# Optimization experiments

Measured on AMD Instinct MI355X. Metric: run time of the kernel, lower is better.

The kernel has to match this reference:

```python
import jax, jax.numpy as jnp
import numpy as np

PAD, EOS, SOS = 0, 1, 2
V, E, H, B, T = 32000, 256, 512, 32, 64


def setup_inputs() -> dict:
    key = jax.random.key(0)
    ks = jax.random.split(key, 8)
    s_e = 1.0 / np.sqrt(H)
    emb = jax.random.normal(ks[0], (V, E), dtype=jnp.float32)
    emb = emb.at[PAD].set(0.0)  # padding_idx=PAD
    return {
        "hidden": jax.random.normal(ks[1], (1, B, H), dtype=jnp.float32),
        "emb": emb,
        "W_ih": jax.random.uniform(ks[2], (3 * H, E), minval=-s_e, maxval=s_e, dtype=jnp.float32),
        "W_hh": jax.random.uniform(ks[3], (3 * H, H), minval=-s_e, maxval=s_e, dtype=jnp.float32),
        "b_ih": jax.random.uniform(ks[4], (3 * H,), minval=-s_e, maxval=s_e, dtype=jnp.float32),
        "b_hh": jax.random.uniform(ks[5], (3 * H,), minval=-s_e, maxval=s_e, dtype=jnp.float32),
        "W_proj": jax.random.uniform(ks[6], (V, H), minval=-s_e, maxval=s_e, dtype=jnp.float32),
        "b_proj": jax.random.uniform(ks[7], (V,), minval=-s_e, maxval=s_e, dtype=jnp.float32),
        "max_len": T,
    }


def reference(hidden, emb, W_ih, W_hh, b_ih, b_hh, W_proj, b_proj, max_len):
    # Batched greedy GRU decode, equivalent to Decodeur.generate:
    # per-step: embed -> GRU cell -> linear proj -> argmax, feed back token.
    h0 = hidden[0]                                  # [B, H]
    nb = h0.shape[0]
    y0 = jnp.full((nb,), SOS, dtype=jnp.int32)
    done0 = jnp.zeros((nb,), dtype=bool)

    def step(carry, _):
        h, y, done = carry
        x = emb[y]                                  # [B, E]
        gx = x @ W_ih.T + b_ih                      # [B, 3H]
        gh = h @ W_hh.T + b_hh                      # [B, 3H]
        gxr, gxz, gxn = jnp.split(gx, 3, axis=-1)
        ghr, ghz, ghn = jnp.split(gh, 3, axis=-1)
        r = jax.nn.sigmoid(gxr + ghr)
        z = jax.nn.sigmoid(gxz + ghz)
        n = jnp.tanh(gxn + r * ghn)
        h_new = (1.0 - z) * n + z * h               # [B, H]
        logits = h_new @ W_proj.T + b_proj          # [B, V]
        y_new = jnp.argmax(logits, axis=-1).astype(jnp.int32)
        tok = jnp.where(done, EOS, y_new)           # pad with EOS once finished
        done_new = done | (y_new == EOS)
        return (h_new, tok, done_new), tok

    _, toks = jax.lax.scan(step, (h0, y0, done0), None, length=max_len)
    return toks                                     # [T, B] int32, EOS-padded
```

## Files before the change

kernel.cpp:

```cpp
#include <hip/hip_runtime.h>
#include <math.h>

#define EOS_TOK 1
#define SOS_TOK 2
#define Bn 32
#define Hn 512
#define En 256
#define Vn 32000
#define G3H 1536
#define NBLK 256
#define NTHR 1024
#define VPB 125
#define GPB 6
#define CE 0.0085f
#define LCAP 2048

typedef unsigned long long ull;
typedef unsigned int uint;
typedef __attribute__((ext_vector_type(8))) __bf16 bf16x8;
typedef __attribute__((ext_vector_type(4))) float f32x4;

union U4B { uint4 u; bf16x8 b; };
__device__ __forceinline__ bf16x8 u2b(uint4 u) { U4B x; x.u = u; return x.b; }

#define WBF_OFF 0ull
#define WN_OFF  32768000ull
#define GH_OFF  32896000ull
#define ES_OFF  33092608ull
#define LBS_OFF 33096704ull
#define DN_OFF  33100800ull
#define H_OFF   33101056ull

struct WS {
    unsigned short* wbf; float* wn; float* gh; ull* es; ull* lbs; int* done; float* h;
};
__device__ __forceinline__ WS get_ws(void* p) {
    WS w;
    w.wbf = (unsigned short*)((char*)p + WBF_OFF);
    w.wn  = (float*)((char*)p + WN_OFF);
    w.gh  = (float*)((char*)p + GH_OFF);
    w.es  = (ull*)((char*)p + ES_OFF);
    w.lbs = (ull*)((char*)p + LBS_OFF);
    w.done= (int*)((char*)p + DN_OFF);
    w.h   = (float*)((char*)p + H_OFF);
    return w;
}

template <typename T>
__device__ __forceinline__ T ldA(const T* p) {
    return __hip_atomic_load(p, __ATOMIC_RELAXED, __HIP_MEMORY_SCOPE_AGENT);
}
template <typename T>
__device__ __forceinline__ void stA(T* p, T v) {
    __hip_atomic_store(p, v, __ATOMIC_RELAXED, __HIP_MEMORY_SCOPE_AGENT);
}

struct PadCnt { ull v; ull pad[7]; };
__device__ PadCnt g_leaf[32];
__device__ ull    g_release;

__device__ __forceinline__ void grid_barrier(int bid) {
    __syncthreads();
    if (threadIdx.x == 0) {
        __builtin_amdgcn_s_waitcnt(0);
        ull my = __hip_atomic_fetch_add(&g_leaf[bid >> 3].v, 1ull,
                                        __ATOMIC_RELAXED, __HIP_MEMORY_SCOPE_AGENT) + 1;
        ull k = (my + 7) >> 3;
        if (bid == 0) {
            ull need = k << 3;
            for (;;) {
                bool again = false;
                #pragma unroll
                for (int i = 0; i < 32; ++i) again |= (ldA(&g_leaf[i].v) < need);
                if (!again) break;
                __builtin_amdgcn_s_sleep(1);
            }
            stA(&g_release, k);
        } else {
            while (ldA(&g_release) < k) __builtin_amdgcn_s_sleep(2);
        }
        __asm__ __volatile__("" ::: "memory");
    }
    __syncthreads();
}

__device__ __forceinline__ uint fkey(float f) {
    uint b = __float_as_uint(f);
    return (b & 0x80000000u) ? ~b : (b | 0x80000000u);
}
__device__ __forceinline__ float ifkey(uint k) {
    uint b = (k & 0x80000000u) ? (k ^ 0x80000000u) : ~k;
    return __uint_as_float(b);
}
__device__ __forceinline__ uint f2bf(float f) {
    uint u = __float_as_uint(f);
    return (u + 0x7FFFu + ((u >> 16) & 1u)) >> 16;
}
__device__ __forceinline__ float bflo(uint u) { return __uint_as_float(u << 16); }
__device__ __forceinline__ float bfhi(uint u) { return __uint_as_float(u & 0xFFFF0000u); }
__device__ __forceinline__ float ulo(ull u) { return __uint_as_float((uint)u); }
__device__ __forceinline__ float uhi(ull u) { return __uint_as_float((uint)(u >> 32)); }

struct SM {
    uint4 h4[2048];
    float hn[32];
    float lbv[32];
    float lbv2[32];
    float ghsc[GPB * 32 * 6];
    ull   red[256];
    int   cnt; int pad0[3];
    unsigned short sidx[LCAP];
    float sU[LCAP];
    int   tok[32];
    float gx[192];
};

__device__ void prologue(int tid, int bid, const float* __restrict__ hidden,
                         const float* __restrict__ W_proj, WS w)
{
    for (int i = bid * NTHR + tid; i < Bn * Hn / 2; i += NBLK * NTHR)
        stA((ull*)w.h + i, ((const ull*)hidden)[i]);
    for (int i = bid * NTHR + tid; i < Vn * Hn / 4; i += NBLK * NTHR) {
        float4 v = ((const float4*)W_proj)[i];
        ull o = (ull)(f2bf(v.x) | (f2bf(v.y) << 16))
              | ((ull)(f2bf(v.z) | (f2bf(v.w) << 16)) << 32);
        stA((ull*)w.wbf + i, o);
    }
    for (int r = bid * NTHR + tid; r < Vn; r += NBLK * NTHR) {
        const float4* wr = (const float4*)(W_proj + (size_t)r * Hn);
        float s0 = 0.f, s1 = 0.f;
        for (int e = 0; e < 128; e += 2) {
            float4 a = wr[e], b4 = wr[e + 1];
            s0 += a.x * a.x + a.z * a.z + b4.x * b4.x + b4.z * b4.z;
            s1 += a.y * a.y + a.w * a.w + b4.y * b4.y + b4.w * b4.w;
        }
        stA(&w.wn[r], sqrtf(s0 + s1) * 1.0005f);
    }
}

__device__ void do_gh(int tid, int bid, const float* __restrict__ W_hh,
                      const float* __restrict__ h, SM* sm)
{
    if (tid < 832) return;
    int idx = tid - 832;
    int b = idx & 31, ks = idx >> 5;
    int f40 = ks * 21 + (ks < 2 ? ks : 2);
    int nf4 = 21 + (ks < 2 ? 1 : 0);
    const ull* hp = (const ull*)h + b * 256 + f40 * 2;
    const float4* wr[GPB];
    #pragma unroll
    for (int r6 = 0; r6 < GPB; ++r6)
        wr[r6] = (const float4*)(W_hh + (size_t)(bid * GPB + r6) * Hn) + f40;
    float p[GPB];
    #pragma unroll
    for (int r6 = 0; r6 < GPB; ++r6) p[r6] = 0.f;
    for (int e = 0; e < nf4; ++e) {
        ull u0 = ldA(hp + 2 * e), u1 = ldA(hp + 2 * e + 1);
        float h0 = ulo(u0), h1 = uhi(u0), h2 = ulo(u1), h3 = uhi(u1);
        #pragma unroll
        for (int r6 = 0; r6 < GPB; ++r6) {
            float4 wv4 = wr[r6][e];
            p[r6] += wv4.x * h0 + wv4.y * h1 + wv4.z * h2 + wv4.w * h3;
        }
    }
    #pragma unroll
    for (int r6 = 0; r6 < GPB; ++r6)
        sm->ghsc[(r6 * 32 + b) * 6 + ks] = p[r6];
}
__device__ void fin_gh(int tid, int base, int bid, const float* __restrict__ b_hh,
                       float* __restrict__ gh, SM* sm)
{
    if (tid >= base && tid < base + 192) {
        int idx = tid - base;
        int r6 = idx >> 5, b = idx & 31;
        float s = 0.f;
        #pragma unroll
        for (int j = 0; j < 6; ++j) s += sm->ghsc[(r6 * 32 + b) * 6 + j];
        int r = bid * GPB + r6;
        stA(&gh[(size_t)b * G3H + r], s + b_hh[r]);
    }
}

__device__ __forceinline__ void phase_bc(int tid, int bid, int t, WS w,
                         const float* __restrict__ W_hh, const float* __restrict__ b_hh,
                         const float* __restrict__ W_proj, const float* __restrict__ b_proj,
                         SM* sm)
{
    for (int i = tid; i < 2048; i += NTHR) {
        int bb = i >> 6, e8 = i & 63;
        const ull* hs = (const ull*)w.h + bb * 256 + e8 * 4;
        ull a = ldA(hs), b2 = ldA(hs + 1), c = ldA(hs + 2), d = ldA(hs + 3);
        uint4 P;
        P.x = f2bf(ulo(a))  | (f2bf(uhi(a))  << 16);
        P.y = f2bf(ulo(b2)) | (f2bf(uhi(b2)) << 16);
        P.z = f2bf(ulo(c))  | (f2bf(uhi(c))  << 16);
        P.w = f2bf(ulo(d))  | (f2bf(uhi(d))  << 16);
        sm->h4[(bb << 6) + (e8 ^ bb)] = P;
    }
    __syncthreads();

    do_gh(tid, bid, W_hh, w.h, sm);

    if (tid >= 800 && tid < 832) {
        int b = tid & 31;
        float s = 0.f;
        for (int e8 = 0; e8 < 64; ++e8) {
            uint4 H = sm->h4[(b << 6) + (e8 ^ b)];
            float f0=bflo(H.x),f1=bfhi(H.x),f2=bflo(H.y),f3=bfhi(H.y);
            float f4=bflo(H.z),f5=bfhi(H.z),f6=bflo(H.w),f7=bfhi(H.w);
            s += f0*f0+f1*f1+f2*f2+f3*f3+f4*f4+f5*f5+f6*f6+f7*f7;
        }
        sm->hn[b] = CE * sqrtf(s);
    }

    const int lane = tid & 63, wv = tid >> 6;
    f32x4 c0 = (f32x4){0.f,0.f,0.f,0.f}, c1 = (f32x4){0.f,0.f,0.f,0.f};
    if (wv < 8) {
        int arow = bid * VPB + wv * 16 + (lane & 15);
        if (arow > Vn - 1) arow = Vn - 1;
        const uint4* wp = (const uint4*)w.wbf + (size_t)arow * 64 + (lane >> 4);
        const int bb0 = lane & 15, bb1 = bb0 + 16;
        const int i0 = bb0 << 6, i1 = bb1 << 6;
        const int eb = lane >> 4;
        #pragma unroll
        for (int ks = 0; ks < 16; ++ks) {
            uint4 av = wp[ks * 4];
            int e8 = ks * 4 + eb;
            uint4 b0 = sm->h4[i0 + (e8 ^ bb0)];
            uint4 b1 = sm->h4[i1 + (e8 ^ bb1)];
            c0 = __builtin_amdgcn_mfma_f32_16x16x32_bf16(u2b(av), u2b(b0), c0, 0, 0, 0);
            c1 = __builtin_amdgcn_mfma_f32_16x16x32_bf16(u2b(av), u2b(b1), c1, 0, 0, 0);
        }
    }
    __syncthreads();

    const int rl0 = wv * 16 + ((lane >> 4) << 2);
    float bp[4], wnr[4];
    if (wv < 8) {
        ull k0 = 0ull, k1 = 0ull;
        const float hn0 = sm->hn[lane & 15], hn1 = sm->hn[(lane & 15) + 16];
        #pragma unroll
        for (int j = 0; j < 4; ++j) {
            int rl = rl0 + j;
            if (rl < VPB) {
                int r = bid * VPB + rl;
                bp[j] = b_proj[r]; wnr[j] = w.wn[r];
                ull q0 = ((ull)fkey(c0[j] + bp[j] - hn0 * wnr[j])) << 32;
                ull q1 = ((ull)fkey(c1[j] + bp[j] - hn1 * wnr[j])) << 32;
                if (q0 > k0) k0 = q0;
                if (q1 > k1) k1 = q1;
            }
        }
        ull o;
        o = __shfl_xor(k0, 16); if (o > k0) k0 = o;
        o = __shfl_xor(k0, 32); if (o > k0) k0 = o;
        o = __shfl_xor(k1, 16); if (o > k1) k1 = o;
        o = __shfl_xor(k1, 32); if (o > k1) k1 = o;
        if (lane < 16) sm->red[(wv << 5) + lane] = k0;
        else if (lane < 32) sm->red[(wv << 5) + 16 + (lane & 15)] = k1;
    }
    __syncthreads();

    if (tid < Bn) {
        ull m = sm->red[tid];
        #pragma unroll
        for (int s = 1; s < 8; ++s) {
            ull v = sm->red[(s << 5) + tid];
            if (v > m) m = v;
        }
        if (m != 0ull)
            atomicMax(&w.lbs[((size_t)(t & 1) * 8 + (bid & 7)) * Bn + tid], m);
        sm->lbv[tid] = (m != 0ull) ? ifkey((uint)(m >> 32)) : -INFINITY;
    }
    if (tid == Bn) sm->cnt = 0;
    __syncthreads();

    if (wv < 8) {
        #pragma unroll
        for (int tile = 0; tile < 2; ++tile) {
            const int b = (lane & 15) + (tile << 4);
            const float hnb = sm->hn[b], lb = sm->lbv[b];
            #pragma unroll
            for (int j = 0; j < 4; ++j) {
                int rl = rl0 + j;
                if (rl < VPB) {
                    float L = (tile ? c1[j] : c0[j]) + bp[j];
                    float U = L + hnb * wnr[j];
                    if (U >= lb) {
                        int ix = atomicAdd(&sm->cnt, 1);
                        if (ix < LCAP) {
                            sm->sidx[ix] = (unsigned short)((rl << 5) | b);
                            sm->sU[ix] = U;
                        }
                    }
                }
            }
        }
    }
    fin_gh(tid, 512, bid, b_hh, w.gh, sm);
    __syncthreads();

    if (tid < Bn) {
        const ull* sl = w.lbs + (size_t)(t & 1) * (8 * Bn);
        ull m = ldA(&sl[tid]);
        #pragma unroll
        for (int s = 1; s < 8; ++s) {
            ull v = ldA(&sl[s * Bn + tid]);
            if (v > m) m = v;
        }
        sm->lbv2[tid] = (m != 0ull) ? ifkey((uint)(m >> 32)) : -INFINITY;
    }
    __syncthreads();

    int nc = sm->cnt;
    if (nc <= LCAP) {
        for (int wi = wv; wi < nc; wi += 16) {
            uint e = sm->sidx[wi];
            int bb = (int)(e & 31);
            if (sm->sU[wi] < sm->lbv2[bb]) continue;
            int r = bid * VPB + (int)(e >> 5);
            const float4* wr = (const float4*)(W_proj + (size_t)r * Hn) + lane * 2;
            float4 wA = wr[0], wB = wr[1];
            const ull* hp = (const ull*)w.h + bb * 256 + lane * 4;
            ull u0 = ldA(hp), u1 = ldA(hp + 1), u2 = ldA(hp + 2), u3 = ldA(hp + 3);
            float s = wA.x*ulo(u0) + wA.y*uhi(u0) + wA.z*ulo(u1) + wA.w*uhi(u1)
                    + wB.x*ulo(u2) + wB.y*uhi(u2) + wB.z*ulo(u3) + wB.w*uhi(u3);
            #pragma unroll
            for (int d = 1; d < 64; d <<= 1) s += __shfl_xor(s, d);
            if (lane == 0) {
                s += b_proj[r];
                ull q = ((ull)fkey(s) << 32) | (uint)(~(uint)r);
                atomicMax(&w.es[((size_t)(t & 1) * 8 + (bid & 7)) * Bn + bb], q);
            }
        }
    } else {
        for (int wi = wv; wi < VPB * Bn; wi += 16) {
            int r = bid * VPB + (wi >> 5), bb = wi & 31;
            const float4* wr = (const float4*)(W_proj + (size_t)r * Hn) + lane * 2;
            float4 wA = wr[0], wB = wr[1];
            const ull* hp = (const ull*)w.h + bb * 256 + lane * 4;
            ull u0 = ldA(hp), u1 = ldA(hp + 1), u2 = ldA(hp + 2), u3 = ldA(hp + 3);
            float s = wA.x*ulo(u0) + wA.y*uhi(u0) + wA.z*ulo(u1) + wA.w*uhi(u1)
                    + wB.x*ulo(u2) + wB.y*uhi(u2) + wB.z*ulo(u3) + wB.w*uhi(u3);
            #pragma unroll
            for (int d = 1; d < 64; d <<= 1) s += __shfl_xor(s, d);
            if (lane == 0) {
                s += b_proj[r];
                ull q = ((ull)fkey(s) << 32) | (uint)(~(uint)r);
                atomicMax(&w.es[((size_t)(t & 1) * 8 + (bid & 7)) * Bn + bb], q);
            }
        }
    }
}

__device__ __forceinline__ void phase_a(int tid, int bid, int t, int T,
                        const float* __restrict__ emb, const float* __restrict__ W_ih,
                        const float* __restrict__ b_ih, WS w, int* __restrict__ out, SM* sm)
{
    float ghr = 0.f, ghz = 0.f, ghn = 0.f;
    const int col_a = bid + ((tid >> 5) << 8);
    if (tid < 64 && t < T) {
        int b = tid & 31;
        const float* ghrow = w.gh + (size_t)b * G3H;
        ghr = ldA(&ghrow[col_a]);
        ghz = ldA(&ghrow[Hn + col_a]);
        ghn = ldA(&ghrow[2 * Hn + col_a]);
    }
    if (tid < Bn) {
        int b = tid, tok, dnew;
        if (t == 0) { tok = SOS_TOK; dnew = 0; }
        else {
            const ull* sl = w.es + (size_t)((t - 1) & 1) * (8 * Bn);
            ull m = ldA(&sl[b]);
            #pragma unroll
            for (int s = 1; s < 8; ++s) {
                ull v = ldA(&sl[s * Bn + b]);
                if (v > m) m = v;
            }
            int idx = (int)(~(uint)m);
            int dold = ldA(&w.done[((t - 1) & 1) * Bn + b]);
            tok = dold ? EOS_TOK : idx;
            dnew = dold | (idx == EOS_TOK);
        }
        sm->tok[b] = tok;
        if (bid == 0) {
            stA(&w.done[(t & 1) * Bn + b], dnew);
            if (t > 0) out[(size_t)(t - 1) * Bn + b] = tok;
            ull* s1 = w.es  + (size_t)(t & 1) * (8 * Bn);
            ull* s2 = w.lbs + (size_t)(t & 1) * (8 * Bn);
            #pragma unroll
            for (int s = 0; s < 8; ++s) { stA(&s1[s * Bn + b], 0ull); stA(&s2[s * Bn + b], 0ull); }
        }
    }
    __syncthreads();
    if (t >= T) return;

    if (tid < 768) {
        int d = tid >> 2, q = tid & 3;
        int b = d & 31, rem = d >> 5, gate = rem >> 1, ci = rem & 1;
        int col = bid + (ci << 8);
        const float* wrow = W_ih + (size_t)(gate * Hn + col) * En + q * (En / 4);
        const float* xrow = emb + (size_t)sm->tok[b] * En + q * (En / 4);
        float ax = 0.f, ay = 0.f;
        #pragma unroll
        for (int e4 = 0; e4 < En / 16; ++e4) {
            float4 w4 = *(const float4*)(wrow + 4 * e4);
            float4 x4 = *(const float4*)(xrow + 4 * e4);
            ax = fmaf(x4.x, w4.x, ax); ay = fmaf(x4.y, w4.y, ay);
            ax = fmaf(x4.z, w4.z, ax); ay = fmaf(x4.w, w4.w, ay);
        }
        float a = ax + ay;
        a += __shfl_xor(a, 1);
        a += __shfl_xor(a, 2);
        if (q == 0) sm->gx[(ci * 3 + gate) * 32 + b] = a;
    }
    __syncthreads();

    if (tid < 64) {
        int b = tid & 31, ci = tid >> 5;
        int col = col_a;
        float gxr = sm->gx[(ci * 3 + 0) * 32 + b] + b_ih[col];
        float gxz = sm->gx[(ci * 3 + 1) * 32 + b] + b_ih[Hn + col];
        float gxn = sm->gx[(ci * 3 + 2) * 32 + b] + b_ih[2 * Hn + col];
        float r = 1.0f / (1.0f + expf(-(gxr + ghr)));
        float z = 1.0f / (1.0f + expf(-(gxz + ghz)));
        float n = tanhf(gxn + r * ghn);
        float* hp = w.h + (size_t)b * Hn + col;
        float hold = ldA(hp);
        stA(hp, (1.0f - z) * n + z * hold);
    }
}

__global__ void __launch_bounds__(NTHR, 4)
decode_coop(const float* __restrict__ hidden, const float* __restrict__ emb,
            const float* __restrict__ W_ih, const float* __restrict__ W_hh,
            const float* __restrict__ b_ih, const float* __restrict__ b_hh,
            const float* __restrict__ W_proj, const float* __restrict__ b_proj,
            const int* __restrict__ max_len_p, int* __restrict__ out, void* ws_raw)
{
    const int tid = threadIdx.x, bid = blockIdx.x;
    __shared__ SM sm;
    WS w = get_ws(ws_raw);
    const int T = max_len_p[0];

    prologue(tid, bid, hidden, W_proj, w);
    grid_barrier(bid);
    do_gh(tid, bid, W_hh, w.h, &sm);
    __syncthreads();
    fin_gh(tid, 0, bid, b_hh, w.gh, &sm);
    grid_barrier(bid);

    for (int t = 0; t < T; ++t) {
        phase_a(tid, bid, t, T, emb, W_ih, b_ih, w, out, &sm);
        grid_barrier(bid);
        phase_bc(tid, bid, t, w, W_hh, b_hh, W_proj, b_proj, &sm);
        grid_barrier(bid);
    }
    phase_a(tid, bid, T, T, emb, W_ih, b_ih, w, out, &sm);
}

__global__ void __launch_bounds__(NTHR, 4)
k_pro(const float* __restrict__ hidden, const float* __restrict__ W_proj, void* ws_raw) {
    WS w = get_ws(ws_raw);
    prologue(threadIdx.x, blockIdx.x, hidden, W_proj, w);
}
__global__ void __launch_bounds__(NTHR, 4)
k_pre(const float* __restrict__ W_hh, const float* __restrict__ b_hh, void* ws_raw) {
    __shared__ SM sm;
    WS w = get_ws(ws_raw);
    do_gh(threadIdx.x, blockIdx.x, W_hh, w.h, &sm);
    __syncthreads();
    fin_gh(threadIdx.x, 0, blockIdx.x, b_hh, w.gh, &sm);
}
__global__ void __launch_bounds__(NTHR, 4)
k_a(int t, const int* __restrict__ max_len_p,
    const float* __restrict__ emb, const float* __restrict__ W_ih,
    const float* __restrict__ b_ih, int* __restrict__ out, void* ws_raw)
{
    int T = max_len_p[0];
    if (t > T) return;
    __shared__ SM sm;
    WS w = get_ws(ws_raw);
    phase_a(threadIdx.x, blockIdx.x, t, T, emb, W_ih, b_ih, w, out, &sm);
}
__global__ void __launch_bounds__(NTHR, 4)
k_bc(int t, const int* __restrict__ max_len_p,
     const float* __restrict__ W_hh, const float* __restrict__ b_hh,
     const float* __restrict__ W_proj, const float* __restrict__ b_proj, void* ws_raw)
{
    if (t >= max_len_p[0]) return;
    __shared__ SM sm;
    WS w = get_ws(ws_raw);
    phase_bc(threadIdx.x, blockIdx.x, t, w, W_hh, b_hh, W_proj, b_proj, &sm);
}

extern "C" void kernel_launch(void* const* d_in, const int* in_sizes, int n_in,
                              void* d_out, int out_size, void* d_ws, size_t ws_size,
                              hipStream_t stream) {
    const float* hidden = (const float*)d_in[0];
    const float* emb    = (const float*)d_in[1];
    const float* W_ih   = (const float*)d_in[2];
    const float* W_hh   = (const float*)d_in[3];
    const float* b_ih   = (const float*)d_in[4];
    const float* b_hh   = (const float*)d_in[5];
    const float* W_proj = (const float*)d_in[6];
    const float* b_proj = (const float*)d_in[7];
    const int* max_len  = (const int*)d_in[8];
    int* out = (int*)d_out;
    void* ws = d_ws;

    void* args[] = {&hidden, &emb, &W_ih, &W_hh, &b_ih, &b_hh,
                    &W_proj, &b_proj, &max_len, &out, &ws};
    hipError_t err = hipLaunchCooperativeKernel((const void*)decode_coop,
                                                dim3(NBLK), dim3(NTHR), args, 0, stream);
    if (err != hipSuccess) {
        (void)hipGetLastError();
        hipLaunchKernelGGL(k_pro, dim3(NBLK), dim3(NTHR), 0, stream, hidden, W_proj, ws);
        hipLaunchKernelGGL(k_pre, dim3(NBLK), dim3(NTHR), 0, stream, W_hh, b_hh, ws);
        for (int t = 0; t <= 64; ++t) {
            hipLaunchKernelGGL(k_a, dim3(NBLK), dim3(NTHR), 0, stream,
                               t, max_len, emb, W_ih, b_ih, out, ws);
            if (t < 64) {
                hipLaunchKernelGGL(k_bc, dim3(NBLK), dim3(NTHR), 0, stream,
                                   t, max_len, W_hh, b_hh, W_proj, b_proj, ws);
            }
        }
    }
}
```

Measured before the change: 4.624 ms.

## Prefetch projection weights before h staging and keep a bf16 copy of h

The GRU update now also writes a bf16 copy of the hidden state into a new workspace buffer, so each step's staging of h into shared memory reads half as many bytes and skips the float-to-bf16 conversion. The bf16 W_proj fragments for the MFMA loop are loaded into registers at the start of the phase, behind a scheduling barrier, so their global latency overlaps the h staging and the W_hh work. This costs 64 extra VGPRs per thread under a launch bound of 4 blocks of 1024 threads, which may cause spills, and adds one 16-bit atomic store per h element.

```diff
diff --git a/kernel.cpp b/kernel.cpp
--- a/kernel.cpp
+++ b/kernel.cpp
@@ -30,9 +30,11 @@
 #define LBS_OFF 33096704ull
 #define DN_OFF  33100800ull
 #define H_OFF   33101056ull
+#define HBF_OFF 33166592ull
 
 struct WS {
     unsigned short* wbf; float* wn; float* gh; ull* es; ull* lbs; int* done; float* h;
+    unsigned short* hbf;
 };
 __device__ __forceinline__ WS get_ws(void* p) {
     WS w;
@@ -43,6 +45,7 @@
     w.lbs = (ull*)((char*)p + LBS_OFF);
     w.done= (int*)((char*)p + DN_OFF);
     w.h   = (float*)((char*)p + H_OFF);
+    w.hbf = (unsigned short*)((char*)p + HBF_OFF);
     return w;
 }
 
@@ -118,8 +121,11 @@
 __device__ void prologue(int tid, int bid, const float* __restrict__ hidden,
                          const float* __restrict__ W_proj, WS w)
 {
-    for (int i = bid * NTHR + tid; i < Bn * Hn / 2; i += NBLK * NTHR)
-        stA((ull*)w.h + i, ((const ull*)hidden)[i]);
+    for (int i = bid * NTHR + tid; i < Bn * Hn / 2; i += NBLK * NTHR) {
+        ull u = ((const ull*)hidden)[i];
+        stA((ull*)w.h + i, u);
+        stA((uint*)w.hbf + i, f2bf(ulo(u)) | (f2bf(uhi(u)) << 16));
+    }
     for (int i = bid * NTHR + tid; i < Vn * Hn / 4; i += NBLK * NTHR) {
         float4 v = ((const float4*)W_proj)[i];
         ull o = (ull)(f2bf(v.x) | (f2bf(v.y) << 16))
@@ -186,15 +192,25 @@
                          const float* __restrict__ W_proj, const float* __restrict__ b_proj,
                          SM* sm)
 {
+    const int lane = tid & 63, wv = tid >> 6;
+
+    uint4 av[16];
+    if (wv < 8) {
+        int arow = bid * VPB + wv * 16 + (lane & 15);
+        if (arow > Vn - 1) arow = Vn - 1;
+        const uint4* wp = (const uint4*)w.wbf + (size_t)arow * 64 + (lane >> 4);
+        #pragma unroll
+        for (int ks = 0; ks < 16; ++ks) av[ks] = wp[ks * 4];
+    }
+    __builtin_amdgcn_sched_barrier(0);
+
     for (int i = tid; i < 2048; i += NTHR) {
         int bb = i >> 6, e8 = i & 63;
-        const ull* hs = (const ull*)w.h + bb * 256 + e8 * 4;
-        ull a = ldA(hs), b2 = ldA(hs + 1), c = ldA(hs + 2), d = ldA(hs + 3);
+        const ull* hs = (const ull*)w.hbf + (size_t)bb * 128 + e8 * 2;
+        ull u0 = ldA(hs), u1 = ldA(hs + 1);
         uint4 P;
-        P.x = f2bf(ulo(a))  | (f2bf(uhi(a))  << 16);
-        P.y = f2bf(ulo(b2)) | (f2bf(uhi(b2)) << 16);
-        P.z = f2bf(ulo(c))  | (f2bf(uhi(c))  << 16);
-        P.w = f2bf(ulo(d))  | (f2bf(uhi(d))  << 16);
+        P.x = (uint)u0; P.y = (uint)(u0 >> 32);
+        P.z = (uint)u1; P.w = (uint)(u1 >> 32);
         sm->h4[(bb << 6) + (e8 ^ bb)] = P;
     }
     __syncthreads();
@@ -213,23 +229,18 @@
         sm->hn[b] = CE * sqrtf(s);
     }
 
-    const int lane = tid & 63, wv = tid >> 6;
     f32x4 c0 = (f32x4){0.f,0.f,0.f,0.f}, c1 = (f32x4){0.f,0.f,0.f,0.f};
     if (wv < 8) {
-        int arow = bid * VPB + wv * 16 + (lane & 15);
-        if (arow > Vn - 1) arow = Vn - 1;
-        const uint4* wp = (const uint4*)w.wbf + (size_t)arow * 64 + (lane >> 4);
         const int bb0 = lane & 15, bb1 = bb0 + 16;
         const int i0 = bb0 << 6, i1 = bb1 << 6;
         const int eb = lane >> 4;
         #pragma unroll
         for (int ks = 0; ks < 16; ++ks) {
-            uint4 av = wp[ks * 4];
             int e8 = ks * 4 + eb;
             uint4 b0 = sm->h4[i0 + (e8 ^ bb0)];
             uint4 b1 = sm->h4[i1 + (e8 ^ bb1)];
-            c0 = __builtin_amdgcn_mfma_f32_16x16x32_bf16(u2b(av), u2b(b0), c0, 0, 0, 0);
-            c1 = __builtin_amdgcn_mfma_f32_16x16x32_bf16(u2b(av), u2b(b1), c1, 0, 0, 0);
+            c0 = __builtin_amdgcn_mfma_f32_16x16x32_bf16(u2b(av[ks]), u2b(b0), c0, 0, 0, 0);
+            c1 = __builtin_amdgcn_mfma_f32_16x16x32_bf16(u2b(av[ks]), u2b(b1), c1, 0, 0, 0);
         }
     }
     __syncthreads();
@@ -427,7 +438,9 @@
         float n = tanhf(gxn + r * ghn);
         float* hp = w.h + (size_t)b * Hn + col;
         float hold = ldA(hp);
-        stA(hp, (1.0f - z) * n + z * hold);
+        float hnew = (1.0f - z) * n + z * hold;
+        stA(hp, hnew);
+        stA(&w.hbf[(size_t)b * Hn + col], (unsigned short)f2bf(hnew));
     }
 }
 
```

Result: slower. 4.950 ms (+7.1%).

## Keep first 80 projection rows per block resident in LDS across decode steps

Applied to the files above, without the earlier changes.

In the cooperative persistent kernel, each block copies the first 80 of its 125 bf16 projection-weight rows into a swizzled LDS buffer once, before the decode loop. The first five waves then read those rows from LDS on every step instead of re-streaming them from global memory, which cuts per-step HBM/L2 traffic. The price is about 80 KB of extra LDS per block (LCAP is halved to make room), which raises LDS pressure and may fail to fit or reduce occupancy. The non-cooperative fallback path keeps reading from global memory.

```diff
diff --git a/kernel.cpp b/kernel.cpp
--- a/kernel.cpp
+++ b/kernel.cpp
@@ -13,7 +13,8 @@
 #define VPB 125
 #define GPB 6
 #define CE 0.0085f
-#define LCAP 2048
+#define LCAP 1024
+#define RRES 80
 
 typedef unsigned long long ull;
 typedef unsigned int uint;
@@ -102,6 +103,7 @@
 __device__ __forceinline__ float uhi(ull u) { return __uint_as_float((uint)(u >> 32)); }
 
 struct SM {
+    uint4 wres[RRES * 64];
     uint4 h4[2048];
     float hn[32];
     float lbv[32];
@@ -135,6 +137,14 @@
             s1 += a.y * a.y + a.w * a.w + b4.y * b4.y + b4.w * b4.w;
         }
         stA(&w.wn[r], sqrtf(s0 + s1) * 1.0005f);
+    }
+}
+
+__device__ __forceinline__ void fill_wres(int tid, int bid, WS w, SM* sm) {
+    const uint4* src = (const uint4*)w.wbf + (size_t)(bid * VPB) * 64;
+    for (int i = tid; i < RRES * 64; i += NTHR) {
+        int rl = i >> 6, c = i & 63;
+        sm->wres[(rl << 6) | (c ^ (rl & 7))] = src[(size_t)rl * 64 + c];
     }
 }
 
@@ -184,7 +194,7 @@
 __device__ __forceinline__ void phase_bc(int tid, int bid, int t, WS w,
                          const float* __restrict__ W_hh, const float* __restrict__ b_hh,
                          const float* __restrict__ W_proj, const float* __restrict__ b_proj,
-                         SM* sm)
+                         SM* sm, bool resident)
 {
     for (int i = tid; i < 2048; i += NTHR) {
         int bb = i >> 6, e8 = i & 63;
@@ -216,20 +226,34 @@
     const int lane = tid & 63, wv = tid >> 6;
     f32x4 c0 = (f32x4){0.f,0.f,0.f,0.f}, c1 = (f32x4){0.f,0.f,0.f,0.f};
     if (wv < 8) {
-        int arow = bid * VPB + wv * 16 + (lane & 15);
-        if (arow > Vn - 1) arow = Vn - 1;
-        const uint4* wp = (const uint4*)w.wbf + (size_t)arow * 64 + (lane >> 4);
         const int bb0 = lane & 15, bb1 = bb0 + 16;
         const int i0 = bb0 << 6, i1 = bb1 << 6;
         const int eb = lane >> 4;
-        #pragma unroll
-        for (int ks = 0; ks < 16; ++ks) {
-            uint4 av = wp[ks * 4];
-            int e8 = ks * 4 + eb;
-            uint4 b0 = sm->h4[i0 + (e8 ^ bb0)];
-            uint4 b1 = sm->h4[i1 + (e8 ^ bb1)];
-            c0 = __builtin_amdgcn_mfma_f32_16x16x32_bf16(u2b(av), u2b(b0), c0, 0, 0, 0);
-            c1 = __builtin_amdgcn_mfma_f32_16x16x32_bf16(u2b(av), u2b(b1), c1, 0, 0, 0);
+        if (resident && wv < 5) {
+            const int rbase = ((wv << 4) + bb0) << 6;
+            const int sw = lane & 7;
+            #pragma unroll
+            for (int ks = 0; ks < 16; ++ks) {
+                uint4 av = sm->wres[rbase | (((ks << 2) | eb) ^ sw)];
+                int e8 = ks * 4 + eb;
+                uint4 b0 = sm->h4[i0 + (e8 ^ bb0)];
+                uint4 b1 = sm->h4[i1 + (e8 ^ bb1)];
+                c0 = __builtin_amdgcn_mfma_f32_16x16x32_bf16(u2b(av), u2b(b0), c0, 0, 0, 0);
+                c1 = __builtin_amdgcn_mfma_f32_16x16x32_bf16(u2b(av), u2b(b1), c1, 0, 0, 0);
+            }
+        } else {
+            int arow = bid * VPB + wv * 16 + bb0;
+            if (arow > Vn - 1) arow = Vn - 1;
+            const uint4* wp = (const uint4*)w.wbf + (size_t)arow * 64 + eb;
+            #pragma unroll
+            for (int ks = 0; ks < 16; ++ks) {
+                uint4 av = wp[ks * 4];
+                int e8 = ks * 4 + eb;
+                uint4 b0 = sm->h4[i0 + (e8 ^ bb0)];
+                uint4 b1 = sm->h4[i1 + (e8 ^ bb1)];
+                c0 = __builtin_amdgcn_mfma_f32_16x16x32_bf16(u2b(av), u2b(b0), c0, 0, 0, 0);
+                c1 = __builtin_amdgcn_mfma_f32_16x16x32_bf16(u2b(av), u2b(b1), c1, 0, 0, 0);
+            }
         }
     }
     __syncthreads();
@@ -445,6 +469,7 @@
 
     prologue(tid, bid, hidden, W_proj, w);
     grid_barrier(bid);
+    fill_wres(tid, bid, w, &sm);
     do_gh(tid, bid, W_hh, w.h, &sm);
     __syncthreads();
     fin_gh(tid, 0, bid, b_hh, w.gh, &sm);
@@ -453,7 +478,7 @@
     for (int t = 0; t < T; ++t) {
         phase_a(tid, bid, t, T, emb, W_ih, b_ih, w, out, &sm);
         grid_barrier(bid);
-        phase_bc(tid, bid, t, w, W_hh, b_hh, W_proj, b_proj, &sm);
+        phase_bc(tid, bid, t, w, W_hh, b_hh, W_proj, b_proj, &sm, true);
         grid_barrier(bid);
     }
     phase_a(tid, bid, T, T, emb, W_ih, b_ih, w, out, &sm);
@@ -491,7 +516,7 @@
     if (t >= max_len_p[0]) return;
     __shared__ SM sm;
     WS w = get_ws(ws_raw);
-    phase_bc(threadIdx.x, blockIdx.x, t, w, W_hh, b_hh, W_proj, b_proj, &sm);
+    phase_bc(threadIdx.x, blockIdx.x, t, w, W_hh, b_hh, W_proj, b_proj, &sm, false);
 }
 
 extern "C" void kernel_launch(void* const* d_in, const int* in_sizes, int n_in,
```

Result: slower. 4.855 ms (+5.0%).
